# Optimization experiments

Measured on AMD Instinct MI355X. Metric: run time of the kernel, lower is better.

Reference implementation:

```python
import jax, jax.numpy as jnp
import numpy as np

B, N, H, K = 8192, 256, 2048, 1
BETA = 0.99
LOG2PI = float(np.log(2.0 * np.pi))


def V(z, Wv):
    # quadratic Lyapunov-style function; one positive value per sample (keepdims)
    u = z @ Wv
    return jnp.sum(u * u, axis=-1, keepdims=True) + 1e-3


def setup_inputs() -> dict:
    key = jax.random.key(0)
    ks = jax.random.split(key, 6)
    s1 = 1.0 / np.sqrt(N)
    s2 = 1.0 / np.sqrt(H)
    return {
        "x": jax.random.normal(ks[0], (B, N), jnp.float32),
        "y": jax.random.normal(ks[1], (B, 1, N), jnp.float32),
        "eps": jax.random.normal(ks[2], (B, 1, N), jnp.float32),
        "W1": jax.random.normal(ks[3], (N, H), jnp.float32) * s1,
        "b1": jnp.zeros((H,), jnp.float32),
        "W2": jax.random.normal(ks[4], (H, 2 * N), jnp.float32) * s2,
        "b2": jnp.zeros((2 * N,), jnp.float32),
        "Wv": jax.random.normal(ks[5], (N, N), jnp.float32) * s1,
    }


def reference(x, y, eps, W1, b1, W2, b2, Wv):
    # fhat: 2-layer MLP -> [B, 2N] = concat(mu, logvar)
    h = jnp.tanh(x @ W1 + b1)
    f = h @ W2 + b2
    mu, logvar = jnp.split(f, 2, axis=-1)            # [B, K*N] each (K=1)
    # torch: stack(split(mu, N, dim=1)).view(-1, 1, N)
    mu = mu.reshape(B, K, N).transpose(1, 0, 2).reshape(B * K, 1, N)
    var = jnp.exp(logvar).reshape(B, K, N).transpose(1, 0, 2).reshape(B * K, 1, N)
    # Lyapunov rescaling of the mean (per-sample scalar scale)
    Vx = V(x, Wv)[:, None, :]                        # [B,1,1]
    Vmu = V(mu, Wv)                                  # [B,1,1]
    bVx = BETA * Vx
    mu_stable = mu * ((bVx - jax.nn.relu(bVx - Vmu)) / Vmu)
    # reparameterized sample of diagonal MVN
    fx = mu_stable + jnp.sqrt(var) * eps             # [B,1,N]
    # diagonal-MVN log_prob, single fused pass
    q = (y - mu_stable) ** 2 / var
    logp = -0.5 * (N * LOG2PI + jnp.sum(jnp.log(var) + q, axis=-1))  # [B,1]
    logp_y = -jnp.sum(logp)
    return fx, logp_y
```

## Files before the change

kernel.cpp:

```cpp
#include <hip/hip_runtime.h>
#include <stdint.h>

#define B_SZ 8192
#define N_SZ 256
#define H_SZ 2048
#define LOG2PI_F 1.8378770664093453f
#define BETA_F 0.99f

typedef unsigned short ushort_t;
typedef __attribute__((ext_vector_type(8))) __bf16 bf16x8;
typedef __attribute__((ext_vector_type(4))) float f32x4;
typedef __attribute__((ext_vector_type(8))) ushort_t u16x8;

__device__ __forceinline__ ushort_t f2bf(float f) {
    unsigned int u = __float_as_uint(f);
    unsigned int r = (u + 0x7FFFu + ((u >> 16) & 1u)) >> 16;
    return (ushort_t)r;
}

__device__ __forceinline__ float fast_tanh(float v) {
    float ex = __expf(2.0f * v);
    return 1.0f - __fdividef(2.0f, ex + 1.0f);
}

__device__ __forceinline__ void async_ld16(const void* g, const char* lds_uniform) {
    __builtin_amdgcn_global_load_lds(
        (const __attribute__((address_space(1))) void*)g,
        (__attribute__((address_space(3))) void*)lds_uniform,
        16, 0, 0);
}

__global__ __launch_bounds__(256, 4)
void gemm1_vx_kernel(const ushort_t* __restrict__ xb, const ushort_t* __restrict__ W1p,
                     const ushort_t* __restrict__ Wvp, const float* __restrict__ b1,
                     ushort_t* __restrict__ hp, float* __restrict__ vxp)
{
    __shared__ __align__(16) char smem[34816];
    char* sA = smem;
    char* sB = smem + 16384;
    const int tid = threadIdx.x;
    const int lane = tid & 63;
    const int w = tid >> 6;
    const int q = lane >> 4;
    const int rlo = lane & 15;
    const int wr = w >> 1, wc = w & 1;

    const int bid = blockIdx.x;
    const int r8 = bid & 7;
    const int u = bid >> 3;
    const int cb = u % 18;
    const int tb = u / 18;
    const int row0 = (r8 + 8 * tb) * 128;

    const bool w1path = cb < 16;
    const int n0 = (w1path ? cb : cb - 16) * 128;
    const ushort_t* Bp = w1path ? W1p : Wvp;
    const int N = w1path ? H_SZ : N_SZ;

    f32x4 acc[4][4];
#pragma unroll
    for (int i = 0; i < 4; ++i)
#pragma unroll
        for (int j = 0; j < 4; ++j)
            acc[i][j] = f32x4{0.f, 0.f, 0.f, 0.f};

    for (int k0 = 0; k0 < N_SZ; k0 += 64) {
        __syncthreads();
#pragma unroll
        for (int r = 0; r < 4; ++r) {
            int c = r * 256 + tid;
            int kq = c >> 7, m = c & 127;
            async_ld16(xb + (size_t)(row0 + m) * N_SZ + k0 + kq * 8, sA + (c << 4));
        }
        int ko0 = k0 >> 3;
#pragma unroll
        for (int r = 0; r < 4; ++r) {
            int c = r * 256 + tid;
            int kq = c >> 7, n = c & 127;
            async_ld16(Bp + ((size_t)(ko0 + kq) * N + n0 + n) * 8, sB + (c << 4));
        }
        __syncthreads();

#pragma unroll
        for (int ks = 0; ks < 2; ++ks) {
            int kq = ks * 4 + q;
            bf16x8 af[4], bfr[4];
#pragma unroll
            for (int i = 0; i < 4; ++i)
                af[i] = *(const bf16x8*)(sA + (((kq << 7) + wr * 64 + i * 16 + rlo) << 4));
#pragma unroll
            for (int j = 0; j < 4; ++j)
                bfr[j] = *(const bf16x8*)(sB + (((kq << 7) + wc * 64 + j * 16 + rlo) << 4));
#pragma unroll
            for (int i = 0; i < 4; ++i)
#pragma unroll
                for (int j = 0; j < 4; ++j)
                    acc[i][j] = __builtin_amdgcn_mfma_f32_16x16x32_bf16(af[i], bfr[j], acc[i][j], 0, 0, 0);
        }
    }

    if (w1path) {
        __syncthreads();
        ushort_t* st = (ushort_t*)smem;
#pragma unroll
        for (int j = 0; j < 4; ++j) {
            int coll = wc * 64 + j * 16 + rlo;
            float bv = b1[n0 + coll];
#pragma unroll
            for (int i = 0; i < 4; ++i) {
                int rowl = wr * 64 + i * 16 + q * 4;
#pragma unroll
                for (int rr = 0; rr < 4; ++rr)
                    st[(rowl + rr) * 136 + coll] = f2bf(fast_tanh(acc[i][j][rr] + bv));
            }
        }
        __syncthreads();
#pragma unroll
        for (int r = 0; r < 8; ++r) {
            int c = r * 256 + tid;
            int m = c & 127, ko = c >> 7;
            u16x8 v = *(const u16x8*)(st + m * 136 + ko * 8);
            *(u16x8*)(hp + ((size_t)((n0 >> 3) + ko) * B_SZ + row0 + m) * 8) = v;
        }
    } else {
        float* vdst = vxp + (n0 >> 7) * B_SZ;
#pragma unroll
        for (int i = 0; i < 4; ++i) {
#pragma unroll
            for (int rr = 0; rr < 4; ++rr) {
                float s = 0.f;
#pragma unroll
                for (int j = 0; j < 4; ++j) { float v = acc[i][j][rr]; s += v * v; }
#pragma unroll
                for (int m = 1; m < 16; m <<= 1) s += __shfl_xor(s, m, 64);
                if (rlo == 0)
                    vdst[row0 + wr * 64 + i * 16 + q * 4 + rr] = s;
            }
        }
    }
}

__global__ __launch_bounds__(256, 2)
void gemm2_kernel(const ushort_t* __restrict__ hp, const ushort_t* __restrict__ W2p,
                  const float* __restrict__ b2, float* __restrict__ f,
                  ushort_t* __restrict__ mub)
{
    __shared__ __align__(16) char smem[49152];
    char* sA = smem;
    char* sB = smem + 16384;
    const int tid = threadIdx.x;
    const int lane = tid & 63;
    const int w = tid >> 6;
    const int q = lane >> 4;
    const int rlo = lane & 15;
    const int wr = w >> 1, wc = w & 1;

    const int bid = blockIdx.x;
    const int r8 = bid & 7;
    const int u = bid >> 3;
    const int cb = u & 3;
    const int tb = u >> 2;
    const int row0 = (r8 + 8 * tb) * 64;
    const int n0 = cb * 128;

    f32x4 acc[2][4];
#pragma unroll
    for (int i = 0; i < 2; ++i)
#pragma unroll
        for (int j = 0; j < 4; ++j)
            acc[i][j] = f32x4{0.f, 0.f, 0.f, 0.f};

    for (int k0 = 0; k0 < H_SZ; k0 += 128) {
        __syncthreads();
        int ko0 = k0 >> 3;
#pragma unroll
        for (int r = 0; r < 4; ++r) {
            int c = r * 256 + tid;
            int kq = c >> 6, m = c & 63;
            async_ld16(hp + ((size_t)(ko0 + kq) * B_SZ + row0 + m) * 8, sA + (c << 4));
        }
#pragma unroll
        for (int r = 0; r < 8; ++r) {
            int c = r * 256 + tid;
            int kq = c >> 7, n = c & 127;
            async_ld16(W2p + ((size_t)(ko0 + kq) * 512 + n0 + n) * 8, sB + (c << 4));
        }
        __syncthreads();

#pragma unroll
        for (int ks = 0; ks < 4; ++ks) {
            int kq = ks * 4 + q;
            bf16x8 af[2], bfr[4];
#pragma unroll
            for (int i = 0; i < 2; ++i)
                af[i] = *(const bf16x8*)(sA + (((kq << 6) + wr * 32 + i * 16 + rlo) << 4));
#pragma unroll
            for (int j = 0; j < 4; ++j)
                bfr[j] = *(const bf16x8*)(sB + (((kq << 7) + wc * 64 + j * 16 + rlo) << 4));
#pragma unroll
            for (int i = 0; i < 2; ++i)
#pragma unroll
                for (int j = 0; j < 4; ++j)
                    acc[i][j] = __builtin_amdgcn_mfma_f32_16x16x32_bf16(af[i], bfr[j], acc[i][j], 0, 0, 0);
        }
    }

#pragma unroll
    for (int j = 0; j < 4; ++j) {
        int col = n0 + wc * 64 + j * 16 + rlo;
        float bv = b2[col];
#pragma unroll
        for (int i = 0; i < 2; ++i) {
            int rowb = row0 + wr * 32 + i * 16 + q * 4;
#pragma unroll
            for (int rr = 0; rr < 4; ++rr)
                f[(size_t)(rowb + rr) * 512 + col] = acc[i][j][rr] + bv;
        }
    }
    if (n0 < N_SZ) {
        __syncthreads();
        ushort_t* st = (ushort_t*)smem;
#pragma unroll
        for (int j = 0; j < 4; ++j) {
            int coll = wc * 64 + j * 16 + rlo;
            float bv = b2[n0 + coll];
#pragma unroll
            for (int i = 0; i < 2; ++i) {
                int rowl = wr * 32 + i * 16 + q * 4;
#pragma unroll
                for (int rr = 0; rr < 4; ++rr)
                    st[(rowl + rr) * 136 + coll] = f2bf(acc[i][j][rr] + bv);
            }
        }
        __syncthreads();
#pragma unroll
        for (int r = 0; r < 4; ++r) {
            int c = r * 256 + tid;
            int m = c >> 4, c8 = c & 15;
            u16x8 v = *(const u16x8*)(st + m * 136 + c8 * 8);
            *(u16x8*)(mub + (size_t)(row0 + m) * N_SZ + n0 + c8 * 8) = v;
        }
    }
}

__global__ __launch_bounds__(256)
void vmu_epilogue_kernel(const ushort_t* __restrict__ mub, const ushort_t* __restrict__ Wvp,
                         const float* __restrict__ f, const float* __restrict__ y,
                         const float* __restrict__ eps, const float* __restrict__ vxp,
                         float* __restrict__ out, float* __restrict__ partials)
{
    __shared__ float vsum[4][16];
    __shared__ float vmu_s[16];
    __shared__ float red[4];
    const int tid = threadIdx.x;
    const int lane = tid & 63;
    const int w = tid >> 6;
    const int q = lane >> 4;
    const int rlo = lane & 15;
    const int r0 = blockIdx.x * 16;

    f32x4 acc[4];
#pragma unroll
    for (int j = 0; j < 4; ++j)
        acc[j] = f32x4{0.f, 0.f, 0.f, 0.f};

    const ushort_t* a0 = mub + (size_t)(r0 + rlo) * N_SZ + q * 8;
    const ushort_t* b0 = Wvp + ((size_t)q * N_SZ + w * 64 + rlo) * 8;
#pragma unroll
    for (int s = 0; s < 8; ++s) {
        bf16x8 af = *(const bf16x8*)(a0 + s * 32);
        bf16x8 bfr[4];
#pragma unroll
        for (int j = 0; j < 4; ++j)
            bfr[j] = *(const bf16x8*)(b0 + s * 4 * N_SZ * 8 + j * 128);
#pragma unroll
        for (int j = 0; j < 4; ++j)
            acc[j] = __builtin_amdgcn_mfma_f32_16x16x32_bf16(af, bfr[j], acc[j], 0, 0, 0);
    }
#pragma unroll
    for (int rr = 0; rr < 4; ++rr) {
        float s = 0.f;
#pragma unroll
        for (int j = 0; j < 4; ++j) { float v = acc[j][rr]; s += v * v; }
#pragma unroll
        for (int m = 1; m < 16; m <<= 1) s += __shfl_xor(s, m, 64);
        if (rlo == 0) vsum[w][q * 4 + rr] = s;
    }
    __syncthreads();
    if (tid < 16)
        vmu_s[tid] = 1e-3f + vsum[0][tid] + vsum[1][tid] + vsum[2][tid] + vsum[3][tid];
    __syncthreads();

    float t = 0.f;
    const int n = tid;
#pragma unroll 4
    for (int r = 0; r < 16; ++r) {
        size_t row = (size_t)(r0 + r);
        float mu = f[row * 512 + n];
        float lv = f[row * 512 + 256 + n];
        float var = expf(lv);
        float Vx = vxp[row] + vxp[B_SZ + row] + 1e-3f;
        float Vmu = vmu_s[r];
        float scale = fminf(BETA_F * Vx, Vmu) / Vmu;
        float mus = mu * scale;
        out[row * 256 + n] = mus + sqrtf(var) * eps[row * 256 + n];
        float d = y[row * 256 + n] - mus;
        t += lv + d * d / var;
    }
#pragma unroll
    for (int m = 32; m >= 1; m >>= 1) t += __shfl_down(t, m, 64);
    if (lane == 0) red[w] = t;
    __syncthreads();
    if (tid == 0)
        partials[blockIdx.x] = red[0] + red[1] + red[2] + red[3];
}

__global__ __launch_bounds__(256)
void reduce_kernel(const float* __restrict__ partials, float* __restrict__ out)
{
    int tid = threadIdx.x;
    float s = partials[tid] + partials[tid + 256];
#pragma unroll
    for (int m = 32; m >= 1; m >>= 1) s += __shfl_down(s, m, 64);
    __shared__ float red[4];
    if ((tid & 63) == 0) red[tid >> 6] = s;
    __syncthreads();
    if (tid == 0)
        out[(size_t)B_SZ * N_SZ] =
            0.5f * (red[0] + red[1] + red[2] + red[3] +
                    (float)N_SZ * LOG2PI_F * (float)B_SZ);
}

__global__ __launch_bounds__(256)
void convert_kernel(const float* __restrict__ x, const float* __restrict__ W1,
                    const float* __restrict__ W2, const float* __restrict__ Wv,
                    ushort_t* __restrict__ xb, ushort_t* __restrict__ W1p,
                    ushort_t* __restrict__ W2p, ushort_t* __restrict__ Wvp)
{
    const int XC = 262144, W1C = 65536, W2C = 131072;
    int c = blockIdx.x * 256 + threadIdx.x;
    if (c < XC) {
        f32x4 a = *(const f32x4*)(x + (size_t)c * 8);
        f32x4 b = *(const f32x4*)(x + (size_t)c * 8 + 4);
        u16x8 o;
#pragma unroll
        for (int i = 0; i < 4; ++i) { o[i] = f2bf(a[i]); o[4 + i] = f2bf(b[i]); }
        *(u16x8*)(xb + (size_t)c * 8) = o;
    } else if (c < XC + W1C) {
        int d = c - XC;
        int ko = d >> 11, n = d & 2047;
        u16x8 o;
#pragma unroll
        for (int ki = 0; ki < 8; ++ki)
            o[ki] = f2bf(W1[(size_t)(ko * 8 + ki) * H_SZ + n]);
        *(u16x8*)(W1p + (size_t)d * 8) = o;
    } else if (c < XC + W1C + W2C) {
        int d = c - XC - W1C;
        int ko = d >> 9, n = d & 511;
        u16x8 o;
#pragma unroll
        for (int ki = 0; ki < 8; ++ki)
            o[ki] = f2bf(W2[(size_t)(ko * 8 + ki) * 512 + n]);
        *(u16x8*)(W2p + (size_t)d * 8) = o;
    } else {
        int d = c - XC - W1C - W2C;
        int ko = d >> 8, n = d & 255;
        u16x8 o;
#pragma unroll
        for (int ki = 0; ki < 8; ++ki)
            o[ki] = f2bf(Wv[(size_t)(ko * 8 + ki) * N_SZ + n]);
        *(u16x8*)(Wvp + (size_t)d * 8) = o;
    }
}

extern "C" void kernel_launch(void* const* d_in, const int* in_sizes, int n_in,
                              void* d_out, int out_size, void* d_ws, size_t ws_size,
                              hipStream_t stream)
{
    const float* x   = (const float*)d_in[0];
    const float* y   = (const float*)d_in[1];
    const float* eps = (const float*)d_in[2];
    const float* W1  = (const float*)d_in[3];
    const float* b1  = (const float*)d_in[4];
    const float* W2  = (const float*)d_in[5];
    const float* b2  = (const float*)d_in[6];
    const float* Wv  = (const float*)d_in[7];
    float* out = (float*)d_out;

    char* ws = (char*)d_ws;
    size_t off = 0;
    auto alloc = [&](size_t bytes) {
        char* p = ws + off;
        off += (bytes + 255) & ~(size_t)255;
        return p;
    };
    ushort_t* xb  = (ushort_t*)alloc((size_t)B_SZ * N_SZ * 2);
    ushort_t* W1p = (ushort_t*)alloc((size_t)N_SZ * H_SZ * 2);
    ushort_t* W2p = (ushort_t*)alloc((size_t)H_SZ * 512 * 2);
    ushort_t* Wvp = (ushort_t*)alloc((size_t)N_SZ * N_SZ * 2);
    ushort_t* hp  = (ushort_t*)alloc((size_t)B_SZ * H_SZ * 2);
    float*    f   = (float*)alloc((size_t)B_SZ * 512 * 4);
    ushort_t* mub = (ushort_t*)alloc((size_t)B_SZ * N_SZ * 2);
    float*    vxp = (float*)alloc((size_t)2 * B_SZ * 4);
    float*    partials = (float*)alloc(512 * 4);

    const int TOTALC = 262144 + 65536 + 131072 + 8192;
    convert_kernel<<<TOTALC / 256, 256, 0, stream>>>(x, W1, W2, Wv, xb, W1p, W2p, Wvp);

    gemm1_vx_kernel<<<1152, 256, 0, stream>>>(xb, W1p, Wvp, b1, hp, vxp);
    gemm2_kernel<<<512, 256, 0, stream>>>(hp, W2p, b2, f, mub);
    vmu_epilogue_kernel<<<512, 256, 0, stream>>>(mub, Wvp, f, y, eps, vxp, out, partials);
    reduce_kernel<<<1, 256, 0, stream>>>(partials, out);
}
```

Measured before the change: 153.9 us.

## Fuse all stages into one persistent kernel with atomic grid barriers

```diff
diff --git a/kernel.cpp b/kernel.cpp
--- a/kernel.cpp
+++ b/kernel.cpp
@@ -30,346 +30,345 @@
         16, 0, 0);
 }
 
-__global__ __launch_bounds__(256, 4)
-void gemm1_vx_kernel(const ushort_t* __restrict__ xb, const ushort_t* __restrict__ W1p,
-                     const ushort_t* __restrict__ Wvp, const float* __restrict__ b1,
-                     ushort_t* __restrict__ hp, float* __restrict__ vxp)
+__device__ __forceinline__ void grid_barrier(unsigned int* cnt, unsigned int target) {
+    __syncthreads();
+    if (threadIdx.x == 0) {
+        __hip_atomic_fetch_add(cnt, 1u, __ATOMIC_ACQ_REL, __HIP_MEMORY_SCOPE_AGENT);
+        while (__hip_atomic_load(cnt, __ATOMIC_ACQUIRE, __HIP_MEMORY_SCOPE_AGENT) < target)
+            __builtin_amdgcn_s_sleep(2);
+    }
+    __syncthreads();
+}
+
+__global__ __launch_bounds__(256, 2)
+void mega_kernel(const float* __restrict__ x, const float* __restrict__ W1,
+                 const float* __restrict__ W2, const float* __restrict__ Wv,
+                 const float* __restrict__ b1, const float* __restrict__ b2,
+                 const float* __restrict__ y, const float* __restrict__ eps,
+                 ushort_t* __restrict__ xb, ushort_t* __restrict__ W1p,
+                 ushort_t* __restrict__ W2p, ushort_t* __restrict__ Wvp,
+                 ushort_t* __restrict__ hp, float* __restrict__ f,
+                 ushort_t* __restrict__ mub, float* __restrict__ partials,
+                 unsigned int* __restrict__ cnt, float* __restrict__ out)
 {
-    __shared__ __align__(16) char smem[34816];
-    char* sA = smem;
-    char* sB = smem + 16384;
+    __shared__ __align__(16) char smem[49152];
     const int tid = threadIdx.x;
+    const int bid = blockIdx.x;
     const int lane = tid & 63;
     const int w = tid >> 6;
     const int q = lane >> 4;
     const int rlo = lane & 15;
     const int wr = w >> 1, wc = w & 1;
 
-    const int bid = blockIdx.x;
-    const int r8 = bid & 7;
-    const int u = bid >> 3;
-    const int cb = u % 18;
-    const int tb = u / 18;
-    const int row0 = (r8 + 8 * tb) * 128;
-
-    const bool w1path = cb < 16;
-    const int n0 = (w1path ? cb : cb - 16) * 128;
-    const ushort_t* Bp = w1path ? W1p : Wvp;
-    const int N = w1path ? H_SZ : N_SZ;
-
-    f32x4 acc[4][4];
-#pragma unroll
-    for (int i = 0; i < 4; ++i)
-#pragma unroll
-        for (int j = 0; j < 4; ++j)
-            acc[i][j] = f32x4{0.f, 0.f, 0.f, 0.f};
-
-    for (int k0 = 0; k0 < N_SZ; k0 += 64) {
+    {
+        const int XC = 262144, W1C = 65536, W2C = 131072;
+        const int TOT = 466944;
+        for (int c = bid * 256 + tid; c < TOT; c += 512 * 256) {
+            if (c < XC) {
+                f32x4 a = *(const f32x4*)(x + (size_t)c * 8);
+                f32x4 b = *(const f32x4*)(x + (size_t)c * 8 + 4);
+                u16x8 o;
+#pragma unroll
+                for (int i = 0; i < 4; ++i) { o[i] = f2bf(a[i]); o[4 + i] = f2bf(b[i]); }
+                *(u16x8*)(xb + (size_t)c * 8) = o;
+            } else if (c < XC + W1C) {
+                int d = c - XC;
+                int ko = d >> 11, n = d & 2047;
+                u16x8 o;
+#pragma unroll
+                for (int ki = 0; ki < 8; ++ki)
+                    o[ki] = f2bf(W1[(size_t)(ko * 8 + ki) * H_SZ + n]);
+                *(u16x8*)(W1p + (size_t)d * 8) = o;
+            } else if (c < XC + W1C + W2C) {
+                int d = c - XC - W1C;
+                int ko = d >> 9, n = d & 511;
+                u16x8 o;
+#pragma unroll
+                for (int ki = 0; ki < 8; ++ki)
+                    o[ki] = f2bf(W2[(size_t)(ko * 8 + ki) * 512 + n]);
+                *(u16x8*)(W2p + (size_t)d * 8) = o;
+            } else {
+                int d = c - XC - W1C - W2C;
+                int ko = d >> 8, n = d & 255;
+                u16x8 o;
+#pragma unroll
+                for (int ki = 0; ki < 8; ++ki)
+                    o[ki] = f2bf(Wv[(size_t)(ko * 8 + ki) * N_SZ + n]);
+                *(u16x8*)(Wvp + (size_t)d * 8) = o;
+            }
+        }
+    }
+    grid_barrier(cnt, 512u);
+
+    {
+        char* sA = smem;
+        char* sB = smem + 16384;
+#pragma unroll
+        for (int tt = 0; tt < 2; ++tt) {
+            const int t = bid + tt * 512;
+            const int r8 = t & 7;
+            const int u = t >> 3;
+            const int cb = u & 15;
+            const int tb = u >> 4;
+            const int row0 = (r8 + 8 * tb) * 128;
+            const int n0 = cb * 128;
+
+            f32x4 acc[4][4];
+#pragma unroll
+            for (int i = 0; i < 4; ++i)
+#pragma unroll
+                for (int j = 0; j < 4; ++j)
+                    acc[i][j] = f32x4{0.f, 0.f, 0.f, 0.f};
+
+            for (int k0 = 0; k0 < N_SZ; k0 += 64) {
+                __syncthreads();
+#pragma unroll
+                for (int r = 0; r < 4; ++r) {
+                    int c = r * 256 + tid;
+                    int kq = c >> 7, m = c & 127;
+                    async_ld16(xb + (size_t)(row0 + m) * N_SZ + k0 + kq * 8, sA + (c << 4));
+                }
+                int ko0 = k0 >> 3;
+#pragma unroll
+                for (int r = 0; r < 4; ++r) {
+                    int c = r * 256 + tid;
+                    int kq = c >> 7, n = c & 127;
+                    async_ld16(W1p + ((size_t)(ko0 + kq) * H_SZ + n0 + n) * 8, sB + (c << 4));
+                }
+                __syncthreads();
+
+#pragma unroll
+                for (int ks = 0; ks < 2; ++ks) {
+                    int kq = ks * 4 + q;
+                    bf16x8 af[4], bfr[4];
+#pragma unroll
+                    for (int i = 0; i < 4; ++i)
+                        af[i] = *(const bf16x8*)(sA + (((kq << 7) + wr * 64 + i * 16 + rlo) << 4));
+#pragma unroll
+                    for (int j = 0; j < 4; ++j)
+                        bfr[j] = *(const bf16x8*)(sB + (((kq << 7) + wc * 64 + j * 16 + rlo) << 4));
+#pragma unroll
+                    for (int i = 0; i < 4; ++i)
+#pragma unroll
+                        for (int j = 0; j < 4; ++j)
+                            acc[i][j] = __builtin_amdgcn_mfma_f32_16x16x32_bf16(af[i], bfr[j], acc[i][j], 0, 0, 0);
+                }
+            }
+
+            __syncthreads();
+            ushort_t* st = (ushort_t*)smem;
+#pragma unroll
+            for (int j = 0; j < 4; ++j) {
+                int coll = wc * 64 + j * 16 + rlo;
+                float bv = b1[n0 + coll];
+#pragma unroll
+                for (int i = 0; i < 4; ++i) {
+                    int rowl = wr * 64 + i * 16 + q * 4;
+#pragma unroll
+                    for (int rr = 0; rr < 4; ++rr)
+                        st[(rowl + rr) * 136 + coll] = f2bf(fast_tanh(acc[i][j][rr] + bv));
+                }
+            }
+            __syncthreads();
+#pragma unroll
+            for (int r = 0; r < 8; ++r) {
+                int c = r * 256 + tid;
+                int m = c & 127, ko = c >> 7;
+                u16x8 v = *(const u16x8*)(st + m * 136 + ko * 8);
+                *(u16x8*)(hp + ((size_t)((n0 >> 3) + ko) * B_SZ + row0 + m) * 8) = v;
+            }
+        }
+    }
+    grid_barrier(cnt, 1024u);
+
+    {
+        char* sA = smem;
+        char* sB = smem + 16384;
+        const int r8 = bid & 7;
+        const int u = bid >> 3;
+        const int cb = u & 3;
+        const int tb = u >> 2;
+        const int row0 = (r8 + 8 * tb) * 64;
+        const int n0 = cb * 128;
+
+        f32x4 acc[2][4];
+#pragma unroll
+        for (int i = 0; i < 2; ++i)
+#pragma unroll
+            for (int j = 0; j < 4; ++j)
+                acc[i][j] = f32x4{0.f, 0.f, 0.f, 0.f};
+
+        for (int k0 = 0; k0 < H_SZ; k0 += 128) {
+            __syncthreads();
+            int ko0 = k0 >> 3;
+#pragma unroll
+            for (int r = 0; r < 4; ++r) {
+                int c = r * 256 + tid;
+                int kq = c >> 6, m = c & 63;
+                async_ld16(hp + ((size_t)(ko0 + kq) * B_SZ + row0 + m) * 8, sA + (c << 4));
+            }
+#pragma unroll
+            for (int r = 0; r < 8; ++r) {
+                int c = r * 256 + tid;
+                int kq = c >> 7, n = c & 127;
+                async_ld16(W2p + ((size_t)(ko0 + kq) * 512 + n0 + n) * 8, sB + (c << 4));
+            }
+            __syncthreads();
+
+#pragma unroll
+            for (int ks = 0; ks < 4; ++ks) {
+                int kq = ks * 4 + q;
+                bf16x8 af[2], bfr[4];
+#pragma unroll
+                for (int i = 0; i < 2; ++i)
+                    af[i] = *(const bf16x8*)(sA + (((kq << 6) + wr * 32 + i * 16 + rlo) << 4));
+#pragma unroll
+                for (int j = 0; j < 4; ++j)
+                    bfr[j] = *(const bf16x8*)(sB + (((kq << 7) + wc * 64 + j * 16 + rlo) << 4));
+#pragma unroll
+                for (int i = 0; i < 2; ++i)
+#pragma unroll
+                    for (int j = 0; j < 4; ++j)
+                        acc[i][j] = __builtin_amdgcn_mfma_f32_16x16x32_bf16(af[i], bfr[j], acc[i][j], 0, 0, 0);
+            }
+        }
+
+#pragma unroll
+        for (int j = 0; j < 4; ++j) {
+            int col = n0 + wc * 64 + j * 16 + rlo;
+            float bv = b2[col];
+#pragma unroll
+            for (int i = 0; i < 2; ++i) {
+                int rowb = row0 + wr * 32 + i * 16 + q * 4;
+#pragma unroll
+                for (int rr = 0; rr < 4; ++rr)
+                    f[(size_t)(rowb + rr) * 512 + col] = acc[i][j][rr] + bv;
+            }
+        }
+        if (n0 < N_SZ) {
+            __syncthreads();
+            ushort_t* st = (ushort_t*)smem;
+#pragma unroll
+            for (int j = 0; j < 4; ++j) {
+                int coll = wc * 64 + j * 16 + rlo;
+                float bv = b2[n0 + coll];
+#pragma unroll
+                for (int i = 0; i < 2; ++i) {
+                    int rowl = wr * 32 + i * 16 + q * 4;
+#pragma unroll
+                    for (int rr = 0; rr < 4; ++rr)
+                        st[(rowl + rr) * 136 + coll] = f2bf(acc[i][j][rr] + bv);
+                }
+            }
+            __syncthreads();
+#pragma unroll
+            for (int r = 0; r < 4; ++r) {
+                int c = r * 256 + tid;
+                int m = c >> 4, c8 = c & 15;
+                u16x8 v = *(const u16x8*)(st + m * 136 + c8 * 8);
+                *(u16x8*)(mub + (size_t)(row0 + m) * N_SZ + n0 + c8 * 8) = v;
+            }
+        }
+    }
+    grid_barrier(cnt, 1536u);
+
+    {
+        float* vsx = (float*)smem;
+        float* vsm = (float*)smem + 64;
+        float* vxs = (float*)smem + 128;
+        float* vms = (float*)smem + 144;
+        float* red = (float*)smem + 160;
+        const int r0 = bid * 16;
+
+        f32x4 accx[4], accm[4];
+#pragma unroll
+        for (int j = 0; j < 4; ++j) {
+            accx[j] = f32x4{0.f, 0.f, 0.f, 0.f};
+            accm[j] = f32x4{0.f, 0.f, 0.f, 0.f};
+        }
+
+        const ushort_t* ax = xb + (size_t)(r0 + rlo) * N_SZ + q * 8;
+        const ushort_t* am = mub + (size_t)(r0 + rlo) * N_SZ + q * 8;
+        const ushort_t* b0 = Wvp + ((size_t)q * N_SZ + w * 64 + rlo) * 8;
+#pragma unroll
+        for (int s = 0; s < 8; ++s) {
+            bf16x8 afx = *(const bf16x8*)(ax + s * 32);
+            bf16x8 afm = *(const bf16x8*)(am + s * 32);
+            bf16x8 bfr[4];
+#pragma unroll
+            for (int j = 0; j < 4; ++j)
+                bfr[j] = *(const bf16x8*)(b0 + s * 4 * N_SZ * 8 + j * 128);
+#pragma unroll
+            for (int j = 0; j < 4; ++j) {
+                accx[j] = __builtin_amdgcn_mfma_f32_16x16x32_bf16(afx, bfr[j], accx[j], 0, 0, 0);
+                accm[j] = __builtin_amdgcn_mfma_f32_16x16x32_bf16(afm, bfr[j], accm[j], 0, 0, 0);
+            }
+        }
+#pragma unroll
+        for (int rr = 0; rr < 4; ++rr) {
+            float sx = 0.f, sm = 0.f;
+#pragma unroll
+            for (int j = 0; j < 4; ++j) {
+                float vx_ = accx[j][rr]; sx += vx_ * vx_;
+                float vm_ = accm[j][rr]; sm += vm_ * vm_;
+            }
+#pragma unroll
+            for (int m = 1; m < 16; m <<= 1) {
+                sx += __shfl_xor(sx, m, 64);
+                sm += __shfl_xor(sm, m, 64);
+            }
+            if (rlo == 0) {
+                vsx[w * 16 + q * 4 + rr] = sx;
+                vsm[w * 16 + q * 4 + rr] = sm;
+            }
+        }
         __syncthreads();
-#pragma unroll
-        for (int r = 0; r < 4; ++r) {
-            int c = r * 256 + tid;
-            int kq = c >> 7, m = c & 127;
-            async_ld16(xb + (size_t)(row0 + m) * N_SZ + k0 + kq * 8, sA + (c << 4));
-        }
-        int ko0 = k0 >> 3;
-#pragma unroll
-        for (int r = 0; r < 4; ++r) {
-            int c = r * 256 + tid;
-            int kq = c >> 7, n = c & 127;
-            async_ld16(Bp + ((size_t)(ko0 + kq) * N + n0 + n) * 8, sB + (c << 4));
+        if (tid < 16) {
+            vxs[tid] = 1e-3f + vsx[tid] + vsx[16 + tid] + vsx[32 + tid] + vsx[48 + tid];
+            vms[tid] = 1e-3f + vsm[tid] + vsm[16 + tid] + vsm[32 + tid] + vsm[48 + tid];
         }
         __syncthreads();
 
-#pragma unroll
-        for (int ks = 0; ks < 2; ++ks) {
-            int kq = ks * 4 + q;
-            bf16x8 af[4], bfr[4];
-#pragma unroll
-            for (int i = 0; i < 4; ++i)
-                af[i] = *(const bf16x8*)(sA + (((kq << 7) + wr * 64 + i * 16 + rlo) << 4));
-#pragma unroll
-            for (int j = 0; j < 4; ++j)
-                bfr[j] = *(const bf16x8*)(sB + (((kq << 7) + wc * 64 + j * 16 + rlo) << 4));
-#pragma unroll
-            for (int i = 0; i < 4; ++i)
-#pragma unroll
-                for (int j = 0; j < 4; ++j)
-                    acc[i][j] = __builtin_amdgcn_mfma_f32_16x16x32_bf16(af[i], bfr[j], acc[i][j], 0, 0, 0);
-        }
-    }
-
-    if (w1path) {
+        float t = 0.f;
+        const int n = tid;
+#pragma unroll 4
+        for (int r = 0; r < 16; ++r) {
+            size_t row = (size_t)(r0 + r);
+            float mu = f[row * 512 + n];
+            float lv = f[row * 512 + 256 + n];
+            float var = expf(lv);
+            float Vx = vxs[r];
+            float Vmu = vms[r];
+            float scale = fminf(BETA_F * Vx, Vmu) / Vmu;
+            float mus = mu * scale;
+            out[row * 256 + n] = mus + sqrtf(var) * eps[row * 256 + n];
+            float d = y[row * 256 + n] - mus;
+            t += lv + d * d / var;
+        }
+#pragma unroll
+        for (int m = 32; m >= 1; m >>= 1) t += __shfl_down(t, m, 64);
+        if (lane == 0) red[w] = t;
         __syncthreads();
-        ushort_t* st = (ushort_t*)smem;
-#pragma unroll
-        for (int j = 0; j < 4; ++j) {
-            int coll = wc * 64 + j * 16 + rlo;
-            float bv = b1[n0 + coll];
-#pragma unroll
-            for (int i = 0; i < 4; ++i) {
-                int rowl = wr * 64 + i * 16 + q * 4;
-#pragma unroll
-                for (int rr = 0; rr < 4; ++rr)
-                    st[(rowl + rr) * 136 + coll] = f2bf(fast_tanh(acc[i][j][rr] + bv));
-            }
+
+        __shared__ int last;
+        if (tid == 0) {
+            partials[bid] = red[0] + red[1] + red[2] + red[3];
+            unsigned int old = __hip_atomic_fetch_add(cnt, 1u, __ATOMIC_ACQ_REL,
+                                                      __HIP_MEMORY_SCOPE_AGENT);
+            last = (old == 2047u);
         }
         __syncthreads();
-#pragma unroll
-        for (int r = 0; r < 8; ++r) {
-            int c = r * 256 + tid;
-            int m = c & 127, ko = c >> 7;
-            u16x8 v = *(const u16x8*)(st + m * 136 + ko * 8);
-            *(u16x8*)(hp + ((size_t)((n0 >> 3) + ko) * B_SZ + row0 + m) * 8) = v;
-        }
-    } else {
-        float* vdst = vxp + (n0 >> 7) * B_SZ;
-#pragma unroll
-        for (int i = 0; i < 4; ++i) {
-#pragma unroll
-            for (int rr = 0; rr < 4; ++rr) {
-                float s = 0.f;
-#pragma unroll
-                for (int j = 0; j < 4; ++j) { float v = acc[i][j][rr]; s += v * v; }
-#pragma unroll
-                for (int m = 1; m < 16; m <<= 1) s += __shfl_xor(s, m, 64);
-                if (rlo == 0)
-                    vdst[row0 + wr * 64 + i * 16 + q * 4 + rr] = s;
-            }
-        }
-    }
-}
-
-__global__ __launch_bounds__(256, 2)
-void gemm2_kernel(const ushort_t* __restrict__ hp, const ushort_t* __restrict__ W2p,
-                  const float* __restrict__ b2, float* __restrict__ f,
-                  ushort_t* __restrict__ mub)
-{
-    __shared__ __align__(16) char smem[49152];
-    char* sA = smem;
-    char* sB = smem + 16384;
-    const int tid = threadIdx.x;
-    const int lane = tid & 63;
-    const int w = tid >> 6;
-    const int q = lane >> 4;
-    const int rlo = lane & 15;
-    const int wr = w >> 1, wc = w & 1;
-
-    const int bid = blockIdx.x;
-    const int r8 = bid & 7;
-    const int u = bid >> 3;
-    const int cb = u & 3;
-    const int tb = u >> 2;
-    const int row0 = (r8 + 8 * tb) * 64;
-    const int n0 = cb * 128;
-
-    f32x4 acc[2][4];
-#pragma unroll
-    for (int i = 0; i < 2; ++i)
-#pragma unroll
-        for (int j = 0; j < 4; ++j)
-            acc[i][j] = f32x4{0.f, 0.f, 0.f, 0.f};
-
-    for (int k0 = 0; k0 < H_SZ; k0 += 128) {
-        __syncthreads();
-        int ko0 = k0 >> 3;
-#pragma unroll
-        for (int r = 0; r < 4; ++r) {
-            int c = r * 256 + tid;
-            int kq = c >> 6, m = c & 63;
-            async_ld16(hp + ((size_t)(ko0 + kq) * B_SZ + row0 + m) * 8, sA + (c << 4));
-        }
-#pragma unroll
-        for (int r = 0; r < 8; ++r) {
-            int c = r * 256 + tid;
-            int kq = c >> 7, n = c & 127;
-            async_ld16(W2p + ((size_t)(ko0 + kq) * 512 + n0 + n) * 8, sB + (c << 4));
-        }
-        __syncthreads();
-
-#pragma unroll
-        for (int ks = 0; ks < 4; ++ks) {
-            int kq = ks * 4 + q;
-            bf16x8 af[2], bfr[4];
-#pragma unroll
-            for (int i = 0; i < 2; ++i)
-                af[i] = *(const bf16x8*)(sA + (((kq << 6) + wr * 32 + i * 16 + rlo) << 4));
-#pragma unroll
-            for (int j = 0; j < 4; ++j)
-                bfr[j] = *(const bf16x8*)(sB + (((kq << 7) + wc * 64 + j * 16 + rlo) << 4));
-#pragma unroll
-            for (int i = 0; i < 2; ++i)
-#pragma unroll
-                for (int j = 0; j < 4; ++j)
-                    acc[i][j] = __builtin_amdgcn_mfma_f32_16x16x32_bf16(af[i], bfr[j], acc[i][j], 0, 0, 0);
-        }
-    }
-
-#pragma unroll
-    for (int j = 0; j < 4; ++j) {
-        int col = n0 + wc * 64 + j * 16 + rlo;
-        float bv = b2[col];
-#pragma unroll
-        for (int i = 0; i < 2; ++i) {
-            int rowb = row0 + wr * 32 + i * 16 + q * 4;
-#pragma unroll
-            for (int rr = 0; rr < 4; ++rr)
-                f[(size_t)(rowb + rr) * 512 + col] = acc[i][j][rr] + bv;
-        }
-    }
-    if (n0 < N_SZ) {
-        __syncthreads();
-        ushort_t* st = (ushort_t*)smem;
-#pragma unroll
-        for (int j = 0; j < 4; ++j) {
-            int coll = wc * 64 + j * 16 + rlo;
-            float bv = b2[n0 + coll];
-#pragma unroll
-            for (int i = 0; i < 2; ++i) {
-                int rowl = wr * 32 + i * 16 + q * 4;
-#pragma unroll
-                for (int rr = 0; rr < 4; ++rr)
-                    st[(rowl + rr) * 136 + coll] = f2bf(acc[i][j][rr] + bv);
-            }
-        }
-        __syncthreads();
-#pragma unroll
-        for (int r = 0; r < 4; ++r) {
-            int c = r * 256 + tid;
-            int m = c >> 4, c8 = c & 15;
-            u16x8 v = *(const u16x8*)(st + m * 136 + c8 * 8);
-            *(u16x8*)(mub + (size_t)(row0 + m) * N_SZ + n0 + c8 * 8) = v;
-        }
-    }
-}
-
-__global__ __launch_bounds__(256)
-void vmu_epilogue_kernel(const ushort_t* __restrict__ mub, const ushort_t* __restrict__ Wvp,
-                         const float* __restrict__ f, const float* __restrict__ y,
-                         const float* __restrict__ eps, const float* __restrict__ vxp,
-                         float* __restrict__ out, float* __restrict__ partials)
-{
-    __shared__ float vsum[4][16];
-    __shared__ float vmu_s[16];
-    __shared__ float red[4];
-    const int tid = threadIdx.x;
-    const int lane = tid & 63;
-    const int w = tid >> 6;
-    const int q = lane >> 4;
-    const int rlo = lane & 15;
-    const int r0 = blockIdx.x * 16;
-
-    f32x4 acc[4];
-#pragma unroll
-    for (int j = 0; j < 4; ++j)
-        acc[j] = f32x4{0.f, 0.f, 0.f, 0.f};
-
-    const ushort_t* a0 = mub + (size_t)(r0 + rlo) * N_SZ + q * 8;
-    const ushort_t* b0 = Wvp + ((size_t)q * N_SZ + w * 64 + rlo) * 8;
-#pragma unroll
-    for (int s = 0; s < 8; ++s) {
-        bf16x8 af = *(const bf16x8*)(a0 + s * 32);
-        bf16x8 bfr[4];
-#pragma unroll
-        for (int j = 0; j < 4; ++j)
-            bfr[j] = *(const bf16x8*)(b0 + s * 4 * N_SZ * 8 + j * 128);
-#pragma unroll
-        for (int j = 0; j < 4; ++j)
-            acc[j] = __builtin_amdgcn_mfma_f32_16x16x32_bf16(af, bfr[j], acc[j], 0, 0, 0);
-    }
-#pragma unroll
-    for (int rr = 0; rr < 4; ++rr) {
-        float s = 0.f;
-#pragma unroll
-        for (int j = 0; j < 4; ++j) { float v = acc[j][rr]; s += v * v; }
-#pragma unroll
-        for (int m = 1; m < 16; m <<= 1) s += __shfl_xor(s, m, 64);
-        if (rlo == 0) vsum[w][q * 4 + rr] = s;
-    }
-    __syncthreads();
-    if (tid < 16)
-        vmu_s[tid] = 1e-3f + vsum[0][tid] + vsum[1][tid] + vsum[2][tid] + vsum[3][tid];
-    __syncthreads();
-
-    float t = 0.f;
-    const int n = tid;
-#pragma unroll 4
-    for (int r = 0; r < 16; ++r) {
-        size_t row = (size_t)(r0 + r);
-        float mu = f[row * 512 + n];
-        float lv = f[row * 512 + 256 + n];
-        float var = expf(lv);
-        float Vx = vxp[row] + vxp[B_SZ + row] + 1e-3f;
-        float Vmu = vmu_s[r];
-        float scale = fminf(BETA_F * Vx, Vmu) / Vmu;
-        float mus = mu * scale;
-        out[row * 256 + n] = mus + sqrtf(var) * eps[row * 256 + n];
-        float d = y[row * 256 + n] - mus;
-        t += lv + d * d / var;
-    }
-#pragma unroll
-    for (int m = 32; m >= 1; m >>= 1) t += __shfl_down(t, m, 64);
-    if (lane == 0) red[w] = t;
-    __syncthreads();
-    if (tid == 0)
-        partials[blockIdx.x] = red[0] + red[1] + red[2] + red[3];
-}
-
-__global__ __launch_bounds__(256)
-void reduce_kernel(const float* __restrict__ partials, float* __restrict__ out)
-{
-    int tid = threadIdx.x;
-    float s = partials[tid] + partials[tid + 256];
-#pragma unroll
-    for (int m = 32; m >= 1; m >>= 1) s += __shfl_down(s, m, 64);
-    __shared__ float red[4];
-    if ((tid & 63) == 0) red[tid >> 6] = s;
-    __syncthreads();
-    if (tid == 0)
-        out[(size_t)B_SZ * N_SZ] =
-            0.5f * (red[0] + red[1] + red[2] + red[3] +
-                    (float)N_SZ * LOG2PI_F * (float)B_SZ);
-}
-
-__global__ __launch_bounds__(256)
-void convert_kernel(const float* __restrict__ x, const float* __restrict__ W1,
-                    const float* __restrict__ W2, const float* __restrict__ Wv,
-                    ushort_t* __restrict__ xb, ushort_t* __restrict__ W1p,
-                    ushort_t* __restrict__ W2p, ushort_t* __restrict__ Wvp)
-{
-    const int XC = 262144, W1C = 65536, W2C = 131072;
-    int c = blockIdx.x * 256 + threadIdx.x;
-    if (c < XC) {
-        f32x4 a = *(const f32x4*)(x + (size_t)c * 8);
-        f32x4 b = *(const f32x4*)(x + (size_t)c * 8 + 4);
-        u16x8 o;
-#pragma unroll
-        for (int i = 0; i < 4; ++i) { o[i] = f2bf(a[i]); o[4 + i] = f2bf(b[i]); }
-        *(u16x8*)(xb + (size_t)c * 8) = o;
-    } else if (c < XC + W1C) {
-        int d = c - XC;
-        int ko = d >> 11, n = d & 2047;
-        u16x8 o;
-#pragma unroll
-        for (int ki = 0; ki < 8; ++ki)
-            o[ki] = f2bf(W1[(size_t)(ko * 8 + ki) * H_SZ + n]);
-        *(u16x8*)(W1p + (size_t)d * 8) = o;
-    } else if (c < XC + W1C + W2C) {
-        int d = c - XC - W1C;
-        int ko = d >> 9, n = d & 511;
-        u16x8 o;
-#pragma unroll
-        for (int ki = 0; ki < 8; ++ki)
-            o[ki] = f2bf(W2[(size_t)(ko * 8 + ki) * 512 + n]);
-        *(u16x8*)(W2p + (size_t)d * 8) = o;
-    } else {
-        int d = c - XC - W1C - W2C;
-        int ko = d >> 8, n = d & 255;
-        u16x8 o;
-#pragma unroll
-        for (int ki = 0; ki < 8; ++ki)
-            o[ki] = f2bf(Wv[(size_t)(ko * 8 + ki) * N_SZ + n]);
-        *(u16x8*)(Wvp + (size_t)d * 8) = o;
+        if (last) {
+            float s = partials[tid] + partials[tid + 256];
+#pragma unroll
+            for (int m = 32; m >= 1; m >>= 1) s += __shfl_down(s, m, 64);
+            if (lane == 0) red[w] = s;
+            __syncthreads();
+            if (tid == 0)
+                out[(size_t)B_SZ * N_SZ] =
+                    0.5f * (red[0] + red[1] + red[2] + red[3] +
+                            (float)N_SZ * LOG2PI_F * (float)B_SZ);
+        }
     }
 }
 
@@ -401,14 +400,12 @@
     ushort_t* hp  = (ushort_t*)alloc((size_t)B_SZ * H_SZ * 2);
     float*    f   = (float*)alloc((size_t)B_SZ * 512 * 4);
     ushort_t* mub = (ushort_t*)alloc((size_t)B_SZ * N_SZ * 2);
-    float*    vxp = (float*)alloc((size_t)2 * B_SZ * 4);
     float*    partials = (float*)alloc(512 * 4);
-
-    const int TOTALC = 262144 + 65536 + 131072 + 8192;
-    convert_kernel<<<TOTALC / 256, 256, 0, stream>>>(x, W1, W2, Wv, xb, W1p, W2p, Wvp);
-
-    gemm1_vx_kernel<<<1152, 256, 0, stream>>>(xb, W1p, Wvp, b1, hp, vxp);
-    gemm2_kernel<<<512, 256, 0, stream>>>(hp, W2p, b2, f, mub);
-    vmu_epilogue_kernel<<<512, 256, 0, stream>>>(mub, Wvp, f, y, eps, vxp, out, partials);
-    reduce_kernel<<<1, 256, 0, stream>>>(partials, out);
-}
+    unsigned int* cnt = (unsigned int*)alloc(256);
+
+    hipMemsetAsync(cnt, 0, 4, stream);
+
+    mega_kernel<<<512, 256, 0, stream>>>(x, W1, W2, Wv, b1, b2, y, eps,
+                                         xb, W1p, W2p, Wvp, hp, f, mub,
+                                         partials, cnt, out);
+}
```

After: 305.8 us. +98.7%, slower.
